# Optimization experiments

Hardware: AMD Instinct MI355X
Metric: run time of the kernel (lower is better)

The kernel has to match this reference:

```python
import jax, jax.numpy as jnp
import numpy as np

EMBED = 768
FFN = 3072
HEADS = 12
HEAD_DIM = EMBED // HEADS
B, T = 4, 2048


def _layer_norm(x, g, b, eps=1e-5):
    m = jnp.mean(x, axis=-1, keepdims=True)
    v = jnp.mean((x - m) ** 2, axis=-1, keepdims=True)
    return (x - m) * jax.lax.rsqrt(v + eps) * g + b


def setup_inputs() -> dict:
    key = jax.random.key(0)
    ks = jax.random.split(key, 8)
    s_e = 1.0 / np.sqrt(EMBED)
    s_f = 1.0 / np.sqrt(FFN)
    # weights stored [in, out] (transpose of torch Linear layout)
    return {
        "x": jax.random.normal(ks[0], (B, T, EMBED), dtype=jnp.float32),
        "ln1_g": jnp.ones((EMBED,), jnp.float32),
        "ln1_b": jnp.zeros((EMBED,), jnp.float32),
        "wq": jax.random.uniform(ks[1], (EMBED, EMBED), jnp.float32, -s_e, s_e),
        "bq": jnp.zeros((EMBED,), jnp.float32),
        "wk": jax.random.uniform(ks[2], (EMBED, EMBED), jnp.float32, -s_e, s_e),
        "bk": jnp.zeros((EMBED,), jnp.float32),
        "wv": jax.random.uniform(ks[3], (EMBED, EMBED), jnp.float32, -s_e, s_e),
        "bv": jnp.zeros((EMBED,), jnp.float32),
        "wo": jax.random.uniform(ks[4], (EMBED, EMBED), jnp.float32, -s_e, s_e),
        "bo": jnp.zeros((EMBED,), jnp.float32),
        "ln2_g": jnp.ones((EMBED,), jnp.float32),
        "ln2_b": jnp.zeros((EMBED,), jnp.float32),
        "w1": jax.random.uniform(ks[5], (EMBED, FFN), jnp.float32, -s_e, s_e),
        "b1": jnp.zeros((FFN,), jnp.float32),
        "w2": jax.random.uniform(ks[6], (FFN, EMBED), jnp.float32, -s_f, s_f),
        "b2": jnp.zeros((EMBED,), jnp.float32),
    }


def reference(x, ln1_g, ln1_b, wq, bq, wk, bk, wv, bv, wo, bo,
              ln2_g, ln2_b, w1, b1, w2, b2):
    Bx, Tx, C = x.shape
    # --- self-attention block (pre-norm) ---
    residual = x
    h = _layer_norm(x, ln1_g, ln1_b)
    q = (h @ wq + bq).reshape(Bx, Tx, HEADS, HEAD_DIM)
    k = (h @ wk + bk).reshape(Bx, Tx, HEADS, HEAD_DIM)
    v = (h @ wv + bv).reshape(Bx, Tx, HEADS, HEAD_DIM)
    scale = 1.0 / np.sqrt(HEAD_DIM)
    attn = jnp.einsum('bqhd,bkhd->bhqk', q, k) * scale  # [B,H,T,T]
    attn = jax.nn.softmax(attn, axis=-1)
    o = jnp.einsum('bhqk,bkhd->bqhd', attn, v).reshape(Bx, Tx, C)
    x = residual + (o @ wo + bo)
    # --- FFN block (pre-norm) ---
    residual = x
    h = _layer_norm(x, ln2_g, ln2_b)
    h = jax.nn.gelu(h @ w1 + b1, approximate=False)
    x = residual + (h @ w2 + b2)
    return x
```

## Files before the change

### kernel.cpp

```cpp
#include <hip/hip_runtime.h>
#include <hip/hip_bf16.h>

#define EMBED 768
#define FFNDIM 3072
#define HEADS 12
#define HDIM  64
#define BB    4
#define TT    2048
#define MTOK  (BB*TT)

typedef __hip_bfloat16 bf16;
typedef __attribute__((ext_vector_type(8))) short short8;
typedef __attribute__((ext_vector_type(4))) float f32x4;
typedef __attribute__((ext_vector_type(16))) float f32x16;
typedef __attribute__((ext_vector_type(4))) unsigned short ushort4v;

__device__ __forceinline__ f32x4 mfma16(short8 a, short8 b, f32x4 c) {
  return __builtin_amdgcn_mfma_f32_16x16x32_bf16(a, b, c, 0, 0, 0);
}
__device__ __forceinline__ f32x16 mfma32(short8 a, short8 b, f32x16 c) {
  return __builtin_amdgcn_mfma_f32_32x32x16_bf16(a, b, c, 0, 0, 0);
}

__device__ __forceinline__ unsigned short f2bf(float f) {
  union { float f; unsigned int u; } v; v.f = f;
  unsigned int u = v.u;
  return (unsigned short)((u + 0x7fffu + ((u >> 16) & 1u)) >> 16);
}

__device__ __forceinline__ float fexp2(float x) {
#if __has_builtin(__builtin_amdgcn_exp2f)
  return __builtin_amdgcn_exp2f(x);
#else
  return exp2f(x);
#endif
}

__device__ __forceinline__ unsigned cvtpk(float lo, float hi) {
  unsigned r;
  asm("v_cvt_pk_bf16_f32 %0, %1, %2" : "=v"(r) : "v"(lo), "v"(hi));
  return r;
}
__device__ __forceinline__ void pl32swap(unsigned& vdst, unsigned& vsrc) {
  asm("v_permlane32_swap_b32 %0, %1" : "+v"(vdst), "+v"(vsrc));
}

__device__ __forceinline__ void gl_lds16(const void* g, void* l) {
  __builtin_amdgcn_global_load_lds((const __attribute__((address_space(1))) void*)g,
                                   (__attribute__((address_space(3))) void*)l, 16, 0, 0);
}

#define QSCALE 0.18033688011112042f
#define DEFER_THR 11.54f

struct TArgs {
  const float* src[6];
  bf16* dst[6];
  int K[6];
  int N[6];
};

__global__ __launch_bounds__(256) void transpose_k(TArgs ta) {
  const int mi = blockIdx.z;
  const int K = ta.K[mi], N = ta.N[mi];
  const int nt = N / 32;
  const int bx = blockIdx.x % nt, by = blockIdx.x / nt;
  const int n0 = bx * 32, k0 = by * 32;
  if (k0 >= K) return;
  __shared__ float t[32][33];
  const float* __restrict__ W = ta.src[mi];
  bf16* __restrict__ Wt = ta.dst[mi];
  const int tx = threadIdx.x & 31, ty = threadIdx.x >> 5;
#pragma unroll
  for (int i = 0; i < 4; ++i) {
    int kk = ty + i * 8;
    t[tx][kk] = W[(size_t)(k0 + kk) * N + n0 + tx];
  }
  __syncthreads();
#pragma unroll
  for (int i = 0; i < 4; ++i) {
    int nn = ty + i * 8;
    Wt[(size_t)(n0 + nn) * K + k0 + tx] = __float2bfloat16(t[nn][tx]);
  }
}

__global__ __launch_bounds__(256) void ln_k(const float* __restrict__ x,
                                            const float* __restrict__ g,
                                            const float* __restrict__ b,
                                            bf16* __restrict__ out) {
  const int row = blockIdx.x * 4 + (threadIdx.x >> 6);
  const int lane = threadIdx.x & 63;
  const float* xr = x + (size_t)row * EMBED;
  float4 v[3];
  float s = 0.f;
#pragma unroll
  for (int i = 0; i < 3; ++i) {
    v[i] = *(const float4*)&xr[i * 256 + lane * 4];
    s += v[i].x + v[i].y + v[i].z + v[i].w;
  }
#pragma unroll
  for (int m = 1; m < 64; m <<= 1) s += __shfl_xor(s, m);
  const float mean = s * (1.f / 768.f);
  float ss = 0.f;
#pragma unroll
  for (int i = 0; i < 3; ++i) {
    float dx = v[i].x - mean, dy = v[i].y - mean, dz = v[i].z - mean, dw = v[i].w - mean;
    ss += dx * dx + dy * dy + dz * dz + dw * dw;
  }
#pragma unroll
  for (int m = 1; m < 64; m <<= 1) ss += __shfl_xor(ss, m);
  const float rstd = rsqrtf(ss * (1.f / 768.f) + 1e-5f);
#pragma unroll
  for (int i = 0; i < 3; ++i) {
    float4 g4 = *(const float4*)&g[i * 256 + lane * 4];
    float4 b4 = *(const float4*)&b[i * 256 + lane * 4];
    ushort4v o4;
    o4[0] = f2bf((v[i].x - mean) * rstd * g4.x + b4.x);
    o4[1] = f2bf((v[i].y - mean) * rstd * g4.y + b4.y);
    o4[2] = f2bf((v[i].z - mean) * rstd * g4.z + b4.z);
    o4[3] = f2bf((v[i].w - mean) * rstd * g4.w + b4.w);
    *(ushort4v*)&out[(size_t)row * EMBED + i * 256 + lane * 4] = o4;
  }
}

template <int EPI, int TN>
__global__ __launch_bounds__(256) void gemm_bt_k(
    const bf16* __restrict__ A, const bf16* __restrict__ Bt,
    const float* __restrict__ bias, const float* __restrict__ bias2,
    const float* __restrict__ bias3, const float* __restrict__ resid,
    float* __restrict__ outf, bf16* __restrict__ outb,
    bf16* __restrict__ outk, bf16* __restrict__ outvt,
    int N, int K) {
  constexpr int MI = (TN == 128) ? 4 : 2;
  const int tid = threadIdx.x;
  const int lane = tid & 63;
  const int w = tid >> 6;
  const int l16 = lane & 15, g = lane >> 4;
  const int wrbase = (TN == 128) ? (w >> 1) * 64 : w * 32;
  const int wcbase = (TN == 128) ? (w & 1) * 64 : 0;

  const int nbx = N / TN;
  const int logical = ((int)blockIdx.x & 7) * ((int)gridDim.x >> 3) + ((int)blockIdx.x >> 3);
  const int m0 = (logical / nbx) * 128, n0 = (logical % nbx) * TN;

  __shared__ bf16 Al[2][128 * 32];
  __shared__ bf16 Bl[2][TN * 32];

  f32x4 acc[MI][4];
#pragma unroll
  for (int i = 0; i < MI; ++i)
#pragma unroll
    for (int j = 0; j < 4; ++j) acc[i][j] = {0.f, 0.f, 0.f, 0.f};

  const int st_r = lane >> 2;
  const int st_c = ((lane & 3) ^ ((lane >> 3) & 3)) * 8;
  const size_t a_base = (size_t)(m0 + w * 32) * K;
  const size_t b_base = (TN == 128) ? (size_t)(n0 + w * 32) * K
                                    : (size_t)(n0 + w * 16) * K;

  auto stage = [&](int bufi, int kt) {
#pragma unroll
    for (int p = 0; p < 2; ++p)
      gl_lds16(A + a_base + (size_t)(p * 16 + st_r) * K + kt + st_c,
               &Al[bufi][(w * 32 + p * 16) * 32]);
    if constexpr (TN == 128) {
#pragma unroll
      for (int p = 0; p < 2; ++p)
        gl_lds16(Bt + b_base + (size_t)(p * 16 + st_r) * K + kt + st_c,
                 &Bl[bufi][(w * 32 + p * 16) * 32]);
    } else {
      gl_lds16(Bt + b_base + (size_t)st_r * K + kt + st_c, &Bl[bufi][(w * 16) * 32]);
    }
  };

  stage(0, 0);
  __syncthreads();
  int buf = 0;
  const int nt = K >> 5;
  const int sw = (l16 >> 1) & 3;
  for (int t = 0; t < nt; ++t) {
    if (t + 1 < nt) stage(buf ^ 1, (t + 1) * 32);
    short8 af[MI], bfr[4];
#pragma unroll
    for (int i = 0; i < MI; ++i)
      af[i] = *(const short8*)&Al[buf][(wrbase + i * 16 + l16) * 32 + (g ^ sw) * 8];
#pragma unroll
    for (int j = 0; j < 4; ++j)
      bfr[j] = *(const short8*)&Bl[buf][(wcbase + j * 16 + l16) * 32 + (g ^ sw) * 8];
#pragma unroll
    for (int i = 0; i < MI; ++i)
#pragma unroll
      for (int j = 0; j < 4; ++j) acc[i][j] = mfma16(af[i], bfr[j], acc[i][j]);
    __syncthreads();
    buf ^= 1;
  }

  const int crow = m0 + wrbase + g * 4;
  const int ccol = n0 + wcbase + l16;

  if constexpr (EPI == 0) {
    const int region = n0 / EMBED;
    const float* bp = (region == 0) ? bias : (region == 1) ? bias2 : bias3;
    if (region < 2) {
      const float sc = (region == 0) ? QSCALE : 1.0f;
      bf16* __restrict__ dst = (region == 0) ? outb : outk;
#pragma unroll
      for (int j = 0; j < 4; ++j) {
        const int cn = ccol - region * EMBED + j * 16;
        const float bvv = bp[cn];
#pragma unroll
        for (int i = 0; i < MI; ++i)
#pragma unroll
          for (int rr = 0; rr < 4; ++rr) {
            const int m = crow + i * 16 + rr;
            dst[(size_t)m * EMBED + cn] = __float2bfloat16((acc[i][j][rr] + bvv) * sc);
          }
      }
    } else {
#pragma unroll
      for (int j = 0; j < 4; ++j) {
        const int cn = ccol - 2 * EMBED + j * 16;
        const float bvv = bp[cn];
        const int hh = cn >> 6, dd = cn & 63;
#pragma unroll
        for (int i = 0; i < MI; ++i) {
          const int m = crow + i * 16;
          const int bb2 = m >> 11, t = m & 2047;
          ushort4v pk;
#pragma unroll
          for (int rr = 0; rr < 4; ++rr) pk[rr] = f2bf(acc[i][j][rr] + bvv);
          *(ushort4v*)&outvt[((size_t)((bb2 * HEADS + hh) * HDIM + dd)) * TT + t] = pk;
        }
      }
    }
  } else if constexpr (EPI == 1) {
#pragma unroll
    for (int j = 0; j < 4; ++j) {
      const int cn = ccol + j * 16;
      const float bvv = bias[cn];
#pragma unroll
      for (int i = 0; i < MI; ++i)
#pragma unroll
        for (int rr = 0; rr < 4; ++rr) {
          const int m = crow + i * 16 + rr;
          const size_t idx = (size_t)m * N + cn;
          outf[idx] = resid[idx] + acc[i][j][rr] + bvv;
        }
    }
  } else {
#pragma unroll
    for (int j = 0; j < 4; ++j) {
      const int cn = ccol + j * 16;
      const float bvv = bias[cn];
#pragma unroll
      for (int i = 0; i < MI; ++i)
#pragma unroll
        for (int rr = 0; rr < 4; ++rr) {
          const int m = crow + i * 16 + rr;
          const float v = acc[i][j][rr] + bvv;
          const float ge = 0.5f * v * (1.f + erff(v * 0.70710678118f));
          outb[(size_t)m * N + cn] = __float2bfloat16(ge);
        }
    }
  }
}

__global__ __launch_bounds__(256) void flash5_k(const bf16* __restrict__ q,
                                                const bf16* __restrict__ k,
                                                const bf16* __restrict__ vt,
                                                bf16* __restrict__ o) {
  const int tid = threadIdx.x, lane = tid & 63;
  const int l32 = lane & 31, hl = lane >> 5;
  const int w = tid >> 6;
  const int logical = ((int)blockIdx.x & 7) * 96 + ((int)blockIdx.x >> 3);
  const int qt = logical & 15;
  const int hb = logical >> 4;
  const int h = hb % HEADS, b = hb / HEADS;
  const int q0 = (qt * 4 + w) * 32;

  __shared__ bf16 Kl[2][64 * 64];
  __shared__ bf16 Vl[2][64 * 64];

  short8 qf[4];
  {
    const bf16* qp = q + (size_t)(b * TT + q0 + l32) * EMBED + h * HDIM + hl * 8;
#pragma unroll
    for (int c = 0; c < 4; ++c) qf[c] = *(const short8*)&qp[c * 16];
  }

  const bf16* __restrict__ kgs = k + (size_t)(b * TT) * EMBED + h * HDIM;
  const bf16* __restrict__ vgs = vt + ((size_t)((b * HEADS + h) * HDIM)) * TT;

  f32x16 oacc0, oacc1;
#pragma unroll
  for (int i = 0; i < 16; ++i) { oacc0[i] = 0.f; oacc1[i] = 0.f; }
  float mrun = -1.0e30f, lrun = 0.f;

  const int st_rw = w * 8 + (lane >> 3);
  const int st_cs0 = lane & 7;
  auto stage = [&](int buf, int kv) {
#pragma unroll
    for (int p = 0; p < 2; ++p) {
      const int r = p * 32 + st_rw;
      const int cs = st_cs0 ^ (r & 7);
      char* kdst = (char*)&Kl[buf][0] + p * 4096 + w * 1024;
      char* vdst = (char*)&Vl[buf][0] + p * 4096 + w * 1024;
      gl_lds16(kgs + (size_t)(kv + r) * EMBED + cs * 8, kdst);
      gl_lds16(vgs + (size_t)r * TT + kv + cs * 8, vdst);
    }
  };

  auto subtile = [&](int buf, int s2) {
    const int krow = s2 * 32 + l32;
    const char* Kb = (const char*)&Kl[buf][0];
    const char* Vb = (const char*)&Vl[buf][0];
    short8 kf[4];
#pragma unroll
    for (int c = 0; c < 4; ++c)
      kf[c] = *(const short8*)(Kb + krow * 128 + (((2 * c + hl) ^ (krow & 7)) * 16));

    f32x16 s;
#pragma unroll
    for (int i = 0; i < 16; ++i) s[i] = 0.f;
    __builtin_amdgcn_s_setprio(1);
#pragma unroll
    for (int c = 0; c < 4; ++c) s = mfma32(kf[c], qf[c], s);
    __builtin_amdgcn_s_setprio(0);

    short8 vf[4];
#pragma unroll
    for (int ks = 0; ks < 2; ++ks)
#pragma unroll
      for (int dc = 0; dc < 2; ++dc) {
        const int vrow = dc * 32 + l32;
        vf[ks * 2 + dc] = *(const short8*)(
            Vb + vrow * 128 + (((s2 * 4 + ks * 2 + hl) ^ (vrow & 7)) * 16));
      }

    float m0 = fmaxf(fmaxf(s[0], s[1]), s[2]);
    float m1 = fmaxf(fmaxf(s[3], s[4]), s[5]);
    float m2 = fmaxf(fmaxf(s[6], s[7]), s[8]);
    float m3 = fmaxf(fmaxf(s[9], s[10]), s[11]);
    float m4 = fmaxf(fmaxf(s[12], s[13]), s[14]);
    float mx = fmaxf(fmaxf(fmaxf(m0, m1), fmaxf(m2, m3)), fmaxf(m4, s[15]));
    mx = fmaxf(mx, __shfl_xor(mx, 32));

    if (!__all(mx <= mrun + DEFER_THR)) {
      const float mn = fmaxf(mrun, mx);
      const float al = fexp2(mrun - mn);
      lrun *= al;
#pragma unroll
      for (int i = 0; i < 16; ++i) { oacc0[i] *= al; oacc1[i] *= al; }
      mrun = mn;
    }

    float p[16];
#pragma unroll
    for (int i = 0; i < 16; ++i) p[i] = fexp2(s[i] - mrun);
    float a8[8];
#pragma unroll
    for (int i = 0; i < 8; ++i) a8[i] = p[2 * i] + p[2 * i + 1];
    float ps = ((a8[0] + a8[1]) + (a8[2] + a8[3])) + ((a8[4] + a8[5]) + (a8[6] + a8[7]));
    ps += __shfl_xor(ps, 32);
    lrun += ps;

    union { unsigned u[4]; short8 s8; } pa0, pa1;
    {
      unsigned U = cvtpk(p[0], p[1]), V = cvtpk(p[4], p[5]);
      pl32swap(V, U); pa0.u[0] = U; pa0.u[2] = V;
      unsigned U1 = cvtpk(p[2], p[3]), V1 = cvtpk(p[6], p[7]);
      pl32swap(V1, U1); pa0.u[1] = U1; pa0.u[3] = V1;
    }
    {
      unsigned U = cvtpk(p[8], p[9]), V = cvtpk(p[12], p[13]);
      pl32swap(V, U); pa1.u[0] = U; pa1.u[2] = V;
      unsigned U1 = cvtpk(p[10], p[11]), V1 = cvtpk(p[14], p[15]);
      pl32swap(V1, U1); pa1.u[1] = U1; pa1.u[3] = V1;
    }

    __builtin_amdgcn_s_setprio(1);
    oacc0 = mfma32(vf[0], pa0.s8, oacc0);
    oacc0 = mfma32(vf[2], pa1.s8, oacc0);
    oacc1 = mfma32(vf[1], pa0.s8, oacc1);
    oacc1 = mfma32(vf[3], pa1.s8, oacc1);
    __builtin_amdgcn_s_setprio(0);
  };

  stage(0, 0);
  __syncthreads();
  int buf = 0;
  const int NT = TT / 64;
  for (int t = 0; t < NT; ++t) {
    if (t + 1 < NT) stage(buf ^ 1, (t + 1) * 64);
    subtile(buf, 0);
    subtile(buf, 1);
    __syncthreads();
    buf ^= 1;
  }

  const float inv = 1.f / lrun;
  bf16* op = o + (size_t)(b * TT + q0 + l32) * EMBED + h * HDIM;
#pragma unroll
  for (int a = 0; a < 4; ++a) {
    ushort4v pk4;
#pragma unroll
    for (int bb = 0; bb < 4; ++bb) pk4[bb] = f2bf(oacc0[a * 4 + bb] * inv);
    *(ushort4v*)&op[a * 8 + hl * 4] = pk4;
#pragma unroll
    for (int bb = 0; bb < 4; ++bb) pk4[bb] = f2bf(oacc1[a * 4 + bb] * inv);
    *(ushort4v*)&op[32 + a * 8 + hl * 4] = pk4;
  }
}

extern "C" void kernel_launch(void* const* d_in, const int* in_sizes, int n_in,
                              void* d_out, int out_size, void* d_ws,
                              size_t ws_size, hipStream_t stream) {
  const float* x = (const float*)d_in[0];
  const float* ln1g = (const float*)d_in[1];
  const float* ln1b = (const float*)d_in[2];
  const float* wq = (const float*)d_in[3];
  const float* bq = (const float*)d_in[4];
  const float* wk = (const float*)d_in[5];
  const float* bk = (const float*)d_in[6];
  const float* wv = (const float*)d_in[7];
  const float* bv = (const float*)d_in[8];
  const float* wo = (const float*)d_in[9];
  const float* bo = (const float*)d_in[10];
  const float* ln2g = (const float*)d_in[11];
  const float* ln2b = (const float*)d_in[12];
  const float* w1 = (const float*)d_in[13];
  const float* b1 = (const float*)d_in[14];
  const float* w2 = (const float*)d_in[15];
  const float* b2 = (const float*)d_in[16];
  float* out = (float*)d_out;

  char* ws = (char*)d_ws;
  size_t off = 0;
  auto alloc = [&](size_t bytes) {
    char* p = ws + off;
    off += (bytes + 255) & ~(size_t)255;
    return p;
  };
  bf16* wqkv_t = (bf16*)alloc((size_t)2304 * 768 * 2);
  bf16* wo_t = (bf16*)alloc((size_t)768 * 768 * 2);
  bf16* w1_t = (bf16*)alloc((size_t)3072 * 768 * 2);
  bf16* w2_t = (bf16*)alloc((size_t)768 * 3072 * 2);
  bf16* h = (bf16*)alloc((size_t)MTOK * EMBED * 2);
  char* qkvo = alloc((size_t)MTOK * EMBED * 2 * 4);
  bf16* qb = (bf16*)qkvo;
  bf16* kb = qb + (size_t)MTOK * EMBED;
  bf16* vtb = kb + (size_t)MTOK * EMBED;
  bf16* ob = vtb + (size_t)MTOK * EMBED;
  bf16* h1 = (bf16*)qkvo;
  float* x1 = (float*)alloc((size_t)MTOK * EMBED * 4);
  (void)ws_size;

  TArgs ta;
  ta.src[0] = wq; ta.dst[0] = wqkv_t;                  ta.K[0] = 768;  ta.N[0] = 768;
  ta.src[1] = wk; ta.dst[1] = wqkv_t + 768 * 768;      ta.K[1] = 768;  ta.N[1] = 768;
  ta.src[2] = wv; ta.dst[2] = wqkv_t + 2 * 768 * 768;  ta.K[2] = 768;  ta.N[2] = 768;
  ta.src[3] = wo; ta.dst[3] = wo_t;                    ta.K[3] = 768;  ta.N[3] = 768;
  ta.src[4] = w1; ta.dst[4] = w1_t;                    ta.K[4] = 768;  ta.N[4] = 3072;
  ta.src[5] = w2; ta.dst[5] = w2_t;                    ta.K[5] = 3072; ta.N[5] = 768;

  transpose_k<<<dim3(2304, 1, 6), dim3(256), 0, stream>>>(ta);
  ln_k<<<dim3(MTOK / 4), dim3(256), 0, stream>>>(x, ln1g, ln1b, h);
  gemm_bt_k<0, 128><<<dim3((2304 / 128) * (MTOK / 128)), dim3(256), 0, stream>>>(
      h, wqkv_t, bq, bk, bv, nullptr, nullptr, qb, kb, vtb, 2304, 768);
  flash5_k<<<dim3(16 * HEADS * BB), dim3(256), 0, stream>>>(qb, kb, vtb, ob);
  gemm_bt_k<1, 64><<<dim3((768 / 64) * (MTOK / 128)), dim3(256), 0, stream>>>(
      ob, wo_t, bo, nullptr, nullptr, x, x1, nullptr, nullptr, nullptr, 768, 768);
  ln_k<<<dim3(MTOK / 4), dim3(256), 0, stream>>>(x1, ln2g, ln2b, h);
  gemm_bt_k<2, 128><<<dim3((3072 / 128) * (MTOK / 128)), dim3(256), 0, stream>>>(
      h, w1_t, b1, nullptr, nullptr, nullptr, nullptr, h1, nullptr, nullptr, 3072, 768);
  gemm_bt_k<1, 64><<<dim3((768 / 64) * (MTOK / 128)), dim3(256), 0, stream>>>(
      h1, w2_t, b2, nullptr, nullptr, x1, out, nullptr, nullptr, nullptr, 768, 3072);
}
```

Before: 317.1 us.

## Triple-buffer LDS staging with vmcnt waits and single barrier per iteration

Both the GEMM and the flash-attention kernels move from double-buffered to triple-buffered LDS tiles. Loads are issued two tiles ahead, and each iteration synchronises with explicit s_waitcnt vmcnt counts plus a single s_barrier, replacing the trailing __syncthreads. The aim is to hide global-to-LDS latency better and halve the barriers per iteration. In exchange it uses more LDS per block, which may lower occupancy, and the hardcoded vmcnt values must match the number of loads each stage issues.

```diff
diff --git a/kernel.cpp b/kernel.cpp
--- a/kernel.cpp
+++ b/kernel.cpp
@@ -48,6 +48,17 @@
 __device__ __forceinline__ void gl_lds16(const void* g, void* l) {
   __builtin_amdgcn_global_load_lds((const __attribute__((address_space(1))) void*)g,
                                    (__attribute__((address_space(3))) void*)l, 16, 0, 0);
+}
+
+template <int N>
+__device__ __forceinline__ void wait_vm() {
+  asm volatile("s_waitcnt vmcnt(%0)" :: "i"(N) : "memory");
+  __builtin_amdgcn_sched_barrier(0);
+}
+__device__ __forceinline__ void block_barrier() {
+  __builtin_amdgcn_sched_barrier(0);
+  __builtin_amdgcn_s_barrier();
+  __builtin_amdgcn_sched_barrier(0);
 }
 
 #define QSCALE 0.18033688011112042f
@@ -132,6 +143,7 @@
     bf16* __restrict__ outk, bf16* __restrict__ outvt,
     int N, int K) {
   constexpr int MI = (TN == 128) ? 4 : 2;
+  constexpr int SN = (TN == 128) ? 4 : 3;
   const int tid = threadIdx.x;
   const int lane = tid & 63;
   const int w = tid >> 6;
@@ -143,8 +155,8 @@
   const int logical = ((int)blockIdx.x & 7) * ((int)gridDim.x >> 3) + ((int)blockIdx.x >> 3);
   const int m0 = (logical / nbx) * 128, n0 = (logical % nbx) * TN;
 
-  __shared__ bf16 Al[2][128 * 32];
-  __shared__ bf16 Bl[2][TN * 32];
+  __shared__ bf16 Al[3][128 * 32];
+  __shared__ bf16 Bl[3][TN * 32];
 
   f32x4 acc[MI][4];
 #pragma unroll
@@ -173,13 +185,18 @@
     }
   };
 
+  const int nt = K >> 5;
   stage(0, 0);
-  __syncthreads();
+  stage(1, 32);
+  const int sw = (l16 >> 1) & 3;
   int buf = 0;
-  const int nt = K >> 5;
-  const int sw = (l16 >> 1) & 3;
   for (int t = 0; t < nt; ++t) {
-    if (t + 1 < nt) stage(buf ^ 1, (t + 1) * 32);
+    if (t < nt - 1) wait_vm<SN>(); else wait_vm<0>();
+    block_barrier();
+    if (t + 2 < nt) {
+      int nb = buf + 2; if (nb >= 3) nb -= 3;
+      stage(nb, (t + 2) * 32);
+    }
     short8 af[MI], bfr[4];
 #pragma unroll
     for (int i = 0; i < MI; ++i)
@@ -191,8 +208,7 @@
     for (int i = 0; i < MI; ++i)
 #pragma unroll
       for (int j = 0; j < 4; ++j) acc[i][j] = mfma16(af[i], bfr[j], acc[i][j]);
-    __syncthreads();
-    buf ^= 1;
+    buf = (buf == 2) ? 0 : buf + 1;
   }
 
   const int crow = m0 + wrbase + g * 4;
@@ -265,7 +281,7 @@
   }
 }
 
-__global__ __launch_bounds__(256) void flash5_k(const bf16* __restrict__ q,
+__global__ __launch_bounds__(256) void flash6_k(const bf16* __restrict__ q,
                                                 const bf16* __restrict__ k,
                                                 const bf16* __restrict__ vt,
                                                 bf16* __restrict__ o) {
@@ -278,8 +294,8 @@
   const int h = hb % HEADS, b = hb / HEADS;
   const int q0 = (qt * 4 + w) * 32;
 
-  __shared__ bf16 Kl[2][64 * 64];
-  __shared__ bf16 Vl[2][64 * 64];
+  __shared__ bf16 Kl[3][64 * 64];
+  __shared__ bf16 Vl[3][64 * 64];
 
   short8 qf[4];
   {
@@ -386,16 +402,20 @@
     __builtin_amdgcn_s_setprio(0);
   };
 
+  const int NT = TT / 64;
   stage(0, 0);
-  __syncthreads();
+  stage(1, 64);
   int buf = 0;
-  const int NT = TT / 64;
   for (int t = 0; t < NT; ++t) {
-    if (t + 1 < NT) stage(buf ^ 1, (t + 1) * 64);
+    if (t < NT - 1) wait_vm<4>(); else wait_vm<0>();
+    block_barrier();
+    if (t + 2 < NT) {
+      int nb = buf + 2; if (nb >= 3) nb -= 3;
+      stage(nb, (t + 2) * 64);
+    }
     subtile(buf, 0);
     subtile(buf, 1);
-    __syncthreads();
-    buf ^= 1;
+    buf = (buf == 2) ? 0 : buf + 1;
   }
 
   const float inv = 1.f / lrun;
@@ -467,7 +487,7 @@
   ln_k<<<dim3(MTOK / 4), dim3(256), 0, stream>>>(x, ln1g, ln1b, h);
   gemm_bt_k<0, 128><<<dim3((2304 / 128) * (MTOK / 128)), dim3(256), 0, stream>>>(
       h, wqkv_t, bq, bk, bv, nullptr, nullptr, qb, kb, vtb, 2304, 768);
-  flash5_k<<<dim3(16 * HEADS * BB), dim3(256), 0, stream>>>(qb, kb, vtb, ob);
+  flash6_k<<<dim3(16 * HEADS * BB), dim3(256), 0, stream>>>(qb, kb, vtb, ob);
   gemm_bt_k<1, 64><<<dim3((768 / 64) * (MTOK / 128)), dim3(256), 0, stream>>>(
       ob, wo_t, bo, nullptr, nullptr, x, x1, nullptr, nullptr, nullptr, 768, 768);
   ln_k<<<dim3(MTOK / 4), dim3(256), 0, stream>>>(x1, ln2g, ln2b, h);
```

Measured after the change: 314.6 us. Within noise of the previous version (-0.8%).
